# Optimization experiments

Hardware: AMD Instinct MI355X
Metric: run time of the kernel (lower is better)

The kernel has to match this reference:

```python
import jax, jax.numpy as jnp
import numpy as np

B = 4           # batchsize == poolsize, pool = arange(B)
N_NODES = 32768
N_EDGES = 262144
CH_V = 16
CH_E = 16
HID = 64
CH_MSG = 2 * CH_V + CH_E  # 48


def setup_inputs() -> dict:
    key = jax.random.key(0)
    ks = jax.random.split(key, 8)
    node_vals = jax.random.normal(ks[0], (B, N_NODES, CH_V), jnp.float32) * 0.01
    edge_vals = jax.random.normal(ks[1], (B, N_EDGES, CH_E), jnp.float32) * 0.1
    conn_a = jax.random.randint(ks[2], (N_EDGES,), 0, N_NODES)
    conn_b = jax.random.randint(ks[3], (N_EDGES,), 0, N_NODES)
    w = lambda k, sh: jax.random.normal(k, sh, jnp.float32) * 0.1
    return {
        "node_vals": node_vals, "edge_vals": edge_vals,
        "conn_a": conn_a, "conn_b": conn_b,
        "Wm1": w(ks[4], (CH_MSG, HID)), "bm1": jnp.zeros((HID,), jnp.float32),
        "Wm2": w(ks[5], (HID, CH_MSG)), "bm2": jnp.zeros((CH_MSG,), jnp.float32),
        "Wu1": w(ks[6], (3 * CH_V, HID)), "bu1": jnp.zeros((HID,), jnp.float32),
        "Wu2": w(ks[7], (HID, CH_V)), "bu2": jnp.zeros((CH_V,), jnp.float32),
    }


def reference(node_vals, edge_vals, conn_a, conn_b,
              Wm1, bm1, Wm2, bm2, Wu1, bu1, Wu2, bu2):
    # NeuralGraph.timestep with node_dropout_p = edge_dropout_p = 0 (masks are identity),
    # use_update=True, average_messages=True, nodes=True, edges=True.
    h_a = node_vals[:, conn_a]                      # [B, E, CH_V] gather at source nodes
    h_b = node_vals[:, conn_b]                      # [B, E, CH_V] gather at target nodes
    h = jnp.concatenate([h_a, h_b, edge_vals], -1)  # [B, E, 48]
    # message MLP (Linear -> tanh -> Linear)
    m = jnp.tanh(h @ Wm1 + bm1) @ Wm2 + bm2         # [B, E, 48]
    m_a = m[..., :CH_V]
    m_b = m[..., CH_V:2 * CH_V]
    m_ab = m[..., 2 * CH_V:]
    # scatter-add aggregation per node (index_add_ along node dim)
    agg_a = jnp.zeros((B, N_NODES, CH_V), m.dtype).at[:, conn_a].add(m_a)
    agg_b = jnp.zeros((B, N_NODES, CH_V), m.dtype).at[:, conn_b].add(m_b)
    # count-based averaging (counts clamped to >= 1, matching the buffer fixup)
    ones = jnp.ones((N_EDGES,), m.dtype)
    cnt_a = jnp.maximum(jax.ops.segment_sum(ones, conn_a, num_segments=N_NODES), 1.0)
    cnt_b = jnp.maximum(jax.ops.segment_sum(ones, conn_b, num_segments=N_NODES), 1.0)
    agg_a = agg_a / cnt_a[None, :, None]
    agg_b = agg_b / cnt_b[None, :, None]
    # update MLP
    u_in = jnp.concatenate([agg_a, agg_b, node_vals], -1)   # [B, N, 48]
    updates = jnp.tanh(u_in @ Wu1 + bu1) @ Wu2 + bu2        # [B, N, CH_V]
    new_node_vals = node_vals + updates
    new_edge_vals = edge_vals + m_ab
    return new_node_vals, new_edge_vals
```

## Files before the change

kernel.cpp:

```cpp
#include <hip/hip_runtime.h>
#include <hip/hip_bf16.h>
#include <cstdint>
#include <cstddef>

#define B 4
#define NN 32768
#define NE 262144
#define CV 16
#define CE 16
#define HID 64
#define CM 48

using frag  = __attribute__((ext_vector_type(8))) short;
using f32x4 = __attribute__((ext_vector_type(4))) float;

__device__ __forceinline__ float fast_tanh(float x) {
    float e = __expf(2.0f * x);
    return 1.0f - 2.0f / (e + 1.0f);
}

__device__ __forceinline__ unsigned short f2bf(float x) {
    union { float f; unsigned u; } v; v.f = x;
    unsigned r = (v.u + 0x7FFFu + ((v.u >> 16) & 1u)) >> 16;
    return (unsigned short)r;
}

__device__ __forceinline__ float bf2f(unsigned short x) {
    union { unsigned u; float f; } v; v.u = ((unsigned)x) << 16;
    return v.f;
}

__device__ __forceinline__ unsigned pk2bf(float lo, float hi) {
    union { __hip_bfloat162 h; unsigned u; } v;
    v.h = __float22bfloat162_rn(make_float2(lo, hi));
    return v.u;
}

__device__ __forceinline__ unsigned swo(int row, int byte_off) {
    return (unsigned)((row << 7) + (byte_off ^ ((row & 7) << 4)));
}

__device__ __forceinline__ void acc8(float* a, uint4 v) {
    a[0] += bf2f((unsigned short)(v.x & 0xFFFFu));
    a[1] += bf2f((unsigned short)(v.x >> 16));
    a[2] += bf2f((unsigned short)(v.y & 0xFFFFu));
    a[3] += bf2f((unsigned short)(v.y >> 16));
    a[4] += bf2f((unsigned short)(v.z & 0xFFFFu));
    a[5] += bf2f((unsigned short)(v.z >> 16));
    a[6] += bf2f((unsigned short)(v.w & 0xFFFFu));
    a[7] += bf2f((unsigned short)(v.w >> 16));
}

__global__ __launch_bounds__(256) void prep_kernel(
    const float* __restrict__ Wm1, const float* __restrict__ bm1,
    const float* __restrict__ Wm2,
    const float* __restrict__ Wu1, const float* __restrict__ bu1,
    const float* __restrict__ Wu2,
    const float* __restrict__ node_vals,
    unsigned short* __restrict__ pW1, unsigned short* __restrict__ pW2,
    unsigned short* __restrict__ pWu1, unsigned short* __restrict__ pWu2,
    unsigned short* __restrict__ nv16)
{
    int i = blockIdx.x * 256 + threadIdx.x;

    {
        int x0 = i * 8;
        const float4* src = (const float4*)(node_vals + x0);
        float4 v0 = src[0], v1 = src[1];
        uint4 o;
        o.x = pk2bf(v0.x, v0.y); o.y = pk2bf(v0.z, v0.w);
        o.z = pk2bf(v1.x, v1.y); o.w = pk2bf(v1.z, v1.w);
        *(uint4*)(nv16 + x0) = o;
    }

    if (blockIdx.x == 0) {
        for (int x = threadIdx.x; x < 4 * 2 * 64 * 8; x += 256) {
            int j = x & 7, lane = (x >> 3) & 63, ks = (x >> 9) & 1, mt = x >> 10;
            int m = mt * 16 + (lane & 15);
            int k = ks * 32 + (lane >> 4) * 8 + j;
            float w = (k < 48) ? Wm1[k * 64 + m] : (k == 48 ? bm1[m] : 0.0f);
            pW1[x] = f2bf(w);
        }
    } else if (blockIdx.x == 1) {
        for (int x = threadIdx.x; x < 3 * 2 * 64 * 8; x += 256) {
            int j = x & 7, lane = (x >> 3) & 63, ks = (x >> 9) & 1, mt = x >> 10;
            int m = mt * 16 + (lane & 15);
            int k = ks * 32 + (lane >> 4) * 8 + j;
            pW2[x] = f2bf(Wm2[k * 48 + m]);
        }
    } else if (blockIdx.x == 2) {
        for (int x = threadIdx.x; x < 4 * 2 * 64 * 8; x += 256) {
            int j = x & 7, lane = (x >> 3) & 63, ks = (x >> 9) & 1, mt = x >> 10;
            int m = mt * 16 + (lane & 15);
            int k = ks * 32 + (lane >> 4) * 8 + j;
            float w = (k < 48) ? Wu1[k * 64 + m] : (k == 48 ? bu1[m] : 0.0f);
            pWu1[x] = f2bf(w);
        }
    } else if (blockIdx.x == 3) {
        for (int x = threadIdx.x; x < 2 * 64 * 8; x += 256) {
            int j = x & 7, lane = (x >> 3) & 63, ks = x >> 9;
            int m = lane & 15;
            int k = ks * 32 + (lane >> 4) * 8 + j;
            pWu2[x] = f2bf(Wu2[k * 16 + m]);
        }
    }
}

__global__ __launch_bounds__(1024) void scan_kernel(
    const int* __restrict__ cnt_a, int* __restrict__ start_a,
    const int* __restrict__ cnt_b, int* __restrict__ start_b)
{
    const int* cnt = (blockIdx.x == 0) ? cnt_a : cnt_b;
    int* start     = (blockIdx.x == 0) ? start_a : start_b;

    __shared__ int sw[16];
    int t = threadIdx.x;
    int lane = t & 63;
    int wv   = t >> 6;
    int base = t * 32;

    int local[32];
    int sum = 0;
    const int4* p = (const int4*)(cnt + base);
#pragma unroll
    for (int q = 0; q < 8; q++) {
        int4 v = p[q];
        local[q*4+0] = v.x; local[q*4+1] = v.y; local[q*4+2] = v.z; local[q*4+3] = v.w;
        sum += v.x + v.y + v.z + v.w;
    }
    int inc = sum;
#pragma unroll
    for (int off = 1; off < 64; off <<= 1) {
        int u = __shfl_up(inc, off);
        if (lane >= off) inc += u;
    }
    if (lane == 63) sw[wv] = inc;
    __syncthreads();
    if (wv == 0 && lane < 16) {
        int v = sw[lane];
        int i2 = v;
#pragma unroll
        for (int off = 1; off < 16; off <<= 1) {
            int u = __shfl_up(i2, off);
            if (lane >= off) i2 += u;
        }
        sw[lane] = i2 - v;
    }
    __syncthreads();

    int run = sw[wv] + inc - sum;
    int4* ps = (int4*)(start + base);
#pragma unroll
    for (int q = 0; q < 8; q++) {
        int4 o;
        o.x = run; run += local[q*4+0];
        o.y = run; run += local[q*4+1];
        o.z = run; run += local[q*4+2];
        o.w = run; run += local[q*4+3];
        ps[q] = o;
    }
}

__global__ __launch_bounds__(256) void eidx_kernel(
    const int* __restrict__ ca, const int* __restrict__ cb,
    const int* __restrict__ rank_a, const int* __restrict__ rank_b,
    const int* __restrict__ start_a, const int* __restrict__ start_b,
    int* __restrict__ eidx_a, int* __restrict__ eidx_b)
{
    int e = blockIdx.x * 256 + threadIdx.x;
    eidx_a[start_a[ca[e]] + rank_a[e]] = e;
    eidx_b[start_b[cb[e]] + rank_b[e]] = e;
}

__global__ __launch_bounds__(256, 5) void edge_kernel(
    const unsigned short* __restrict__ nv16, const float* __restrict__ edge_vals,
    const int* __restrict__ ca, const int* __restrict__ cb,
    int* __restrict__ cnt_a, int* __restrict__ cnt_b,
    int* __restrict__ rank_a, int* __restrict__ rank_b,
    const unsigned short* __restrict__ pW1, const unsigned short* __restrict__ pW2,
    const float* __restrict__ bm2,
    float* __restrict__ out_edge,
    unsigned short* __restrict__ ma, unsigned short* __restrict__ mb)
{
    __shared__ unsigned short sH[256 * 64];
    char* sB = (char*)sH;

    int t    = threadIdx.x;
    int lane = t & 63;
    int col  = lane & 15;
    int quad = lane >> 4;
    int erow = (t >> 6) * 64;
    int cha  = quad * 4;

    size_t eb  = (size_t)blockIdx.x * 256;
    size_t idx = eb + t;
    int e  = (int)(idx & (NE - 1));
    int bb = (int)(idx >> 18);

    int na = ca[e], nb = cb[e];

    if (bb == 0) {
        rank_a[e] = atomicAdd(&cnt_a[na], 1);
        rank_b[e] = atomicAdd(&cnt_b[nb], 1);
    }

    {
        const uint4* gA = (const uint4*)(nv16 + ((size_t)bb * NN + na) * CV);
        const uint4* gB = (const uint4*)(nv16 + ((size_t)bb * NN + nb) * CV);
        uint4 a0 = gA[0], a1 = gA[1];
        uint4 b0 = gB[0], b1 = gB[1];
        const float4* pE = (const float4*)(edge_vals + idx * CE);
        float4 ev0 = pE[0], ev1 = pE[1], ev2 = pE[2], ev3 = pE[3];

        unsigned pk[32];
        *(uint4*)&pk[0]  = a0;  *(uint4*)&pk[4]  = a1;
        *(uint4*)&pk[8]  = b0;  *(uint4*)&pk[12] = b1;
        pk[16] = pk2bf(ev0.x, ev0.y); pk[17] = pk2bf(ev0.z, ev0.w);
        pk[18] = pk2bf(ev1.x, ev1.y); pk[19] = pk2bf(ev1.z, ev1.w);
        pk[20] = pk2bf(ev2.x, ev2.y); pk[21] = pk2bf(ev2.z, ev2.w);
        pk[22] = pk2bf(ev3.x, ev3.y); pk[23] = pk2bf(ev3.z, ev3.w);
        pk[24] = 0x3F80u;
#pragma unroll
        for (int q = 25; q < 32; q++) pk[q] = 0;
        const uint4* src = (const uint4*)pk;
#pragma unroll
        for (int q = 0; q < 8; q++)
            *(uint4*)(sB + swo(t, q * 16)) = src[q];
    }
    asm volatile("s_waitcnt lgkmcnt(0)" ::: "memory");

#pragma unroll
    for (int hh = 0; hh < 2; hh++) {
        int r0 = erow + hh * 32 + col;

        frag w1f[4][2];
#pragma unroll
        for (int mt = 0; mt < 4; mt++)
#pragma unroll
            for (int ks = 0; ks < 2; ks++)
                w1f[mt][ks] = *(const frag*)&pW1[(((mt * 2 + ks) * 64) + lane) * 8];

        f32x4 acc1[4][2];
#pragma unroll
        for (int mt = 0; mt < 4; mt++)
#pragma unroll
            for (int n = 0; n < 2; n++) acc1[mt][n] = (f32x4){0.f, 0.f, 0.f, 0.f};

#pragma unroll
        for (int ks = 0; ks < 2; ks++) {
            frag bfr[2];
#pragma unroll
            for (int n = 0; n < 2; n++)
                bfr[n] = *(const frag*)(sB + swo(r0 + n * 16, ks * 64 + quad * 16));
#pragma unroll
            for (int mt = 0; mt < 4; mt++)
#pragma unroll
                for (int n = 0; n < 2; n++)
                    acc1[mt][n] = __builtin_amdgcn_mfma_f32_16x16x32_bf16(
                        w1f[mt][ks], bfr[n], acc1[mt][n], 0, 0, 0);
        }

#pragma unroll
        for (int n = 0; n < 2; n++) {
            int row = r0 + n * 16;
#pragma unroll
            for (int mt = 0; mt < 4; mt++) {
                uint2 w;
                w.x = pk2bf(fast_tanh(acc1[mt][n][0]), fast_tanh(acc1[mt][n][1]));
                w.y = pk2bf(fast_tanh(acc1[mt][n][2]), fast_tanh(acc1[mt][n][3]));
                *(uint2*)(sB + swo(row, mt * 32 + quad * 8)) = w;
            }
        }
        asm volatile("s_waitcnt lgkmcnt(0)" ::: "memory");

        frag w2f[3][2];
#pragma unroll
        for (int mt = 0; mt < 3; mt++)
#pragma unroll
            for (int ks = 0; ks < 2; ks++)
                w2f[mt][ks] = *(const frag*)&pW2[(((mt * 2 + ks) * 64) + lane) * 8];

        f32x4 acc2[3][2];
#pragma unroll
        for (int mt = 0; mt < 3; mt++)
#pragma unroll
            for (int n = 0; n < 2; n++) acc2[mt][n] = (f32x4){0.f, 0.f, 0.f, 0.f};

#pragma unroll
        for (int ks = 0; ks < 2; ks++) {
            frag bfr[2];
#pragma unroll
            for (int n = 0; n < 2; n++)
                bfr[n] = *(const frag*)(sB + swo(r0 + n * 16, ks * 64 + quad * 16));
#pragma unroll
            for (int mt = 0; mt < 3; mt++)
#pragma unroll
                for (int n = 0; n < 2; n++)
                    acc2[mt][n] = __builtin_amdgcn_mfma_f32_16x16x32_bf16(
                        w2f[mt][ks], bfr[n], acc2[mt][n], 0, 0, 0);
        }

        float4 b2e = *(const float4*)&bm2[32 + cha];
#pragma unroll
        for (int n = 0; n < 2; n++) {
            int le = r0 + n * 16;
            size_t o = (eb + le) * CE + cha;
            float4 evv = *(const float4*)&edge_vals[o];
            float4 ov;
            ov.x = evv.x + acc2[2][n][0] + b2e.x;
            ov.y = evv.y + acc2[2][n][1] + b2e.y;
            ov.z = evv.z + acc2[2][n][2] + b2e.z;
            ov.w = evv.w + acc2[2][n][3] + b2e.w;
            *(float4*)&out_edge[o] = ov;
        }

        float4 b2a = *(const float4*)&bm2[cha];
        float4 b2b = *(const float4*)&bm2[16 + cha];
#pragma unroll
        for (int n = 0; n < 2; n++) {
            int row = r0 + n * 16;
            uint2 wa;
            wa.x = pk2bf(acc2[0][n][0] + b2a.x, acc2[0][n][1] + b2a.y);
            wa.y = pk2bf(acc2[0][n][2] + b2a.z, acc2[0][n][3] + b2a.w);
            *(uint2*)(sB + swo(row, quad * 8)) = wa;
            uint2 wb;
            wb.x = pk2bf(acc2[1][n][0] + b2b.x, acc2[1][n][1] + b2b.y);
            wb.y = pk2bf(acc2[1][n][2] + b2b.z, acc2[1][n][3] + b2b.w);
            *(uint2*)(sB + swo(row, 32 + quad * 8)) = wb;
        }
    }
    asm volatile("s_waitcnt lgkmcnt(0)" ::: "memory");

    {
        uint4 a0 = *(const uint4*)(sB + swo(t, 0));
        uint4 a1 = *(const uint4*)(sB + swo(t, 16));
        uint4 b0 = *(const uint4*)(sB + swo(t, 32));
        uint4 b1 = *(const uint4*)(sB + swo(t, 48));
        unsigned short* pa = &ma[idx * 16];
        *(uint4*)(pa + 0) = a0;
        *(uint4*)(pa + 8) = a1;
        unsigned short* pb = &mb[idx * 16];
        *(uint4*)(pb + 0) = b0;
        *(uint4*)(pb + 8) = b1;
    }
}

__global__ __launch_bounds__(256, 4) void node_kernel(
    const float* __restrict__ node_vals,
    const unsigned short* __restrict__ ma, const unsigned short* __restrict__ mb,
    const int* __restrict__ eidx_a, const int* __restrict__ eidx_b,
    const int* __restrict__ start_a, const int* __restrict__ start_b,
    const int* __restrict__ cnt_a, const int* __restrict__ cnt_b,
    const unsigned short* __restrict__ pWu1, const unsigned short* __restrict__ pWu2,
    const float* __restrict__ bu2,
    float* __restrict__ out_node)
{
    __shared__ unsigned short sH[256 * 64];
    char* sB = (char*)sH;

    int t    = threadIdx.x;
    int lane = t & 63;
    int col  = lane & 15;
    int quad = lane >> 4;
    int erow = (t >> 6) * 64;

    int g = blockIdx.x * 256 + t;
    int n = g & (NN - 1);
    int b = g >> 15;

    float4 pn[4];
    {
        float ua[16] = {0.f,0.f,0.f,0.f,0.f,0.f,0.f,0.f,0.f,0.f,0.f,0.f,0.f,0.f,0.f,0.f};
        float ub[16] = {0.f,0.f,0.f,0.f,0.f,0.f,0.f,0.f,0.f,0.f,0.f,0.f,0.f,0.f,0.f,0.f};
        int da = cnt_a[n], sa = start_a[n];
        int db = cnt_b[n], sbn = start_b[n];
        const int* ia = eidx_a + sa;
        const int* ib = eidx_b + sbn;
        const unsigned short* mab = ma + (size_t)b * NE * 16;
        const unsigned short* mbb = mb + (size_t)b * NE * 16;
        for (int k = 0; k < da; k++) {
            int ee = ia[k];
            const uint4* p = (const uint4*)(mab + (size_t)ee * 16);
            acc8(&ua[0], p[0]);
            acc8(&ua[8], p[1]);
        }
        for (int k = 0; k < db; k++) {
            int ee = ib[k];
            const uint4* p = (const uint4*)(mbb + (size_t)ee * 16);
            acc8(&ub[0], p[0]);
            acc8(&ub[8], p[1]);
        }
        float inva = 1.0f / (float)max(da, 1);
        float invb = 1.0f / (float)max(db, 1);

        const float4* pnv = (const float4*)(node_vals + (size_t)g * CV);
#pragma unroll
        for (int q = 0; q < 4; q++) pn[q] = pnv[q];

        unsigned pk[32];
#pragma unroll
        for (int q = 0; q < 8; q++)
            pk[q] = pk2bf(ua[2*q] * inva, ua[2*q+1] * inva);
#pragma unroll
        for (int q = 0; q < 8; q++)
            pk[8 + q] = pk2bf(ub[2*q] * invb, ub[2*q+1] * invb);
#pragma unroll
        for (int q = 0; q < 4; q++) {
            pk[16 + 2*q + 0] = pk2bf(pn[q].x, pn[q].y);
            pk[16 + 2*q + 1] = pk2bf(pn[q].z, pn[q].w);
        }
        pk[24] = 0x3F80u;
#pragma unroll
        for (int q = 25; q < 32; q++) pk[q] = 0;
        const uint4* src = (const uint4*)pk;
#pragma unroll
        for (int q = 0; q < 8; q++)
            *(uint4*)(sB + swo(t, q * 16)) = src[q];
    }
    asm volatile("s_waitcnt lgkmcnt(0)" ::: "memory");

#pragma unroll
    for (int hh = 0; hh < 2; hh++) {
        int r0 = erow + hh * 32 + col;

        frag w1f[4][2];
#pragma unroll
        for (int mt = 0; mt < 4; mt++)
#pragma unroll
            for (int ks = 0; ks < 2; ks++)
                w1f[mt][ks] = *(const frag*)&pWu1[(((mt * 2 + ks) * 64) + lane) * 8];

        f32x4 acc1[4][2];
#pragma unroll
        for (int mt = 0; mt < 4; mt++)
#pragma unroll
            for (int nt = 0; nt < 2; nt++) acc1[mt][nt] = (f32x4){0.f, 0.f, 0.f, 0.f};

#pragma unroll
        for (int ks = 0; ks < 2; ks++) {
            frag bfr[2];
#pragma unroll
            for (int nt = 0; nt < 2; nt++)
                bfr[nt] = *(const frag*)(sB + swo(r0 + nt * 16, ks * 64 + quad * 16));
#pragma unroll
            for (int mt = 0; mt < 4; mt++)
#pragma unroll
                for (int nt = 0; nt < 2; nt++)
                    acc1[mt][nt] = __builtin_amdgcn_mfma_f32_16x16x32_bf16(
                        w1f[mt][ks], bfr[nt], acc1[mt][nt], 0, 0, 0);
        }

#pragma unroll
        for (int nt = 0; nt < 2; nt++) {
            int row = r0 + nt * 16;
#pragma unroll
            for (int mt = 0; mt < 4; mt++) {
                uint2 w;
                w.x = pk2bf(fast_tanh(acc1[mt][nt][0]), fast_tanh(acc1[mt][nt][1]));
                w.y = pk2bf(fast_tanh(acc1[mt][nt][2]), fast_tanh(acc1[mt][nt][3]));
                *(uint2*)(sB + swo(row, mt * 32 + quad * 8)) = w;
            }
        }
        asm volatile("s_waitcnt lgkmcnt(0)" ::: "memory");

        frag w2f[2];
#pragma unroll
        for (int ks = 0; ks < 2; ks++)
            w2f[ks] = *(const frag*)&pWu2[(ks * 64 + lane) * 8];

        f32x4 acc2[2];
#pragma unroll
        for (int nt = 0; nt < 2; nt++) acc2[nt] = (f32x4){0.f, 0.f, 0.f, 0.f};

#pragma unroll
        for (int ks = 0; ks < 2; ks++) {
            frag bfr[2];
#pragma unroll
            for (int nt = 0; nt < 2; nt++)
                bfr[nt] = *(const frag*)(sB + swo(r0 + nt * 16, ks * 64 + quad * 16));
#pragma unroll
            for (int nt = 0; nt < 2; nt++)
                acc2[nt] = __builtin_amdgcn_mfma_f32_16x16x32_bf16(
                    w2f[ks], bfr[nt], acc2[nt], 0, 0, 0);
        }

#pragma unroll
        for (int nt = 0; nt < 2; nt++) {
            int row = r0 + nt * 16;
            float4 v;
            v.x = acc2[nt][0]; v.y = acc2[nt][1];
            v.z = acc2[nt][2]; v.w = acc2[nt][3];
            *(float4*)(sB + swo(row, 64 + quad * 16)) = v;
        }
    }
    asm volatile("s_waitcnt lgkmcnt(0)" ::: "memory");

    {
        const float4* pb2 = (const float4*)bu2;
        float4* po = (float4*)&out_node[(size_t)g * CV];
#pragma unroll
        for (int q = 0; q < 4; q++) {
            float4 m = *(const float4*)(sB + swo(t, 64 + q * 16));
            float4 c = pb2[q];
            float4 o;
            o.x = pn[q].x + m.x + c.x;
            o.y = pn[q].y + m.y + c.y;
            o.z = pn[q].z + m.z + c.z;
            o.w = pn[q].w + m.w + c.w;
            po[q] = o;
        }
    }
}

extern "C" void kernel_launch(void* const* d_in, const int* in_sizes, int n_in,
                              void* d_out, int out_size, void* d_ws, size_t ws_size,
                              hipStream_t stream) {
    const float* node_vals = (const float*)d_in[0];
    const float* edge_vals = (const float*)d_in[1];
    const int*   ca        = (const int*)d_in[2];
    const int*   cb        = (const int*)d_in[3];
    const float* Wm1 = (const float*)d_in[4];
    const float* bm1 = (const float*)d_in[5];
    const float* Wm2 = (const float*)d_in[6];
    const float* bm2 = (const float*)d_in[7];
    const float* Wu1 = (const float*)d_in[8];
    const float* bu1 = (const float*)d_in[9];
    const float* Wu2 = (const float*)d_in[10];
    const float* bu2 = (const float*)d_in[11];

    float* out_node = (float*)d_out;
    float* out_edge = out_node + (size_t)B * NN * CV;

    unsigned short* ma = (unsigned short*)d_ws;
    unsigned short* mb = ma + (size_t)B * NE * 16;
    int* cnt_a   = (int*)(mb + (size_t)B * NE * 16);
    int* cnt_b   = cnt_a + NN;
    int* start_a = cnt_b + NN;
    int* start_b = start_a + NN;
    int* rank_a  = start_b + NN;
    int* rank_b  = rank_a + NE;
    int* eidx_a  = rank_b + NE;
    int* eidx_b  = eidx_a + NE;
    unsigned short* pW1  = (unsigned short*)(eidx_b + NE);
    unsigned short* pW2  = pW1 + 4096;
    unsigned short* pWu1 = pW2 + 3072;
    unsigned short* pWu2 = pWu1 + 4096;
    unsigned short* nv16 = pWu2 + 1024;

    hipMemsetAsync(cnt_a, 0, 2 * (size_t)NN * sizeof(int), stream);

    prep_kernel<<<NE / 256, 256, 0, stream>>>(
        Wm1, bm1, Wm2, Wu1, bu1, Wu2, node_vals,
        pW1, pW2, pWu1, pWu2, nv16);
    edge_kernel<<<(B * NE) / 256, 256, 0, stream>>>(
        nv16, edge_vals, ca, cb, cnt_a, cnt_b, rank_a, rank_b,
        pW1, pW2, bm2, out_edge, ma, mb);
    scan_kernel<<<2, 1024, 0, stream>>>(cnt_a, start_a, cnt_b, start_b);
    eidx_kernel<<<NE / 256, 256, 0, stream>>>(
        ca, cb, rank_a, rank_b, start_a, start_b, eidx_a, eidx_b);
    node_kernel<<<(B * NN) / 256, 256, 0, stream>>>(
        node_vals, ma, mb, eidx_a, eidx_b, start_a, start_b, cnt_a, cnt_b,
        pWu1, pWu2, bu2, out_node);
}
```

Measured before the change: 288.6 us.

## Interleave batch in message buffers and map batches to waves per edge block

Moves the per-node degree counting and rank atomics out of the edge kernel into the prep kernel. Each edge block now covers 64 edges with one wave per batch, so the four batch copies share the ca/cb index loads. Message buffers switch to an edge-major, batch-interleaved layout, and node-kernel threads cover four batches of one node. The four threads gathering a node's messages therefore read one contiguous 128-byte span per edge instead of four scattered ones. The trade-off is more scattered node-value gathers per wave and a reordered kernel sequence.

```diff
diff --git a/kernel.cpp b/kernel.cpp
--- a/kernel.cpp
+++ b/kernel.cpp
@@ -51,7 +51,10 @@
     a[7] += bf2f((unsigned short)(v.w >> 16));
 }
 
-__global__ __launch_bounds__(256) void prep_kernel(
+__global__ __launch_bounds__(256) void count_kernel(
+    const int* __restrict__ ca, const int* __restrict__ cb,
+    int* __restrict__ cnt_a, int* __restrict__ cnt_b,
+    int* __restrict__ rank_a, int* __restrict__ rank_b,
     const float* __restrict__ Wm1, const float* __restrict__ bm1,
     const float* __restrict__ Wm2,
     const float* __restrict__ Wu1, const float* __restrict__ bu1,
@@ -62,6 +65,8 @@
     unsigned short* __restrict__ nv16)
 {
     int i = blockIdx.x * 256 + threadIdx.x;
+    rank_a[i] = atomicAdd(&cnt_a[ca[i]], 1);
+    rank_b[i] = atomicAdd(&cnt_b[cb[i]], 1);
 
     {
         int x0 = i * 8;
@@ -175,8 +180,6 @@
 __global__ __launch_bounds__(256, 5) void edge_kernel(
     const unsigned short* __restrict__ nv16, const float* __restrict__ edge_vals,
     const int* __restrict__ ca, const int* __restrict__ cb,
-    int* __restrict__ cnt_a, int* __restrict__ cnt_b,
-    int* __restrict__ rank_a, int* __restrict__ rank_b,
     const unsigned short* __restrict__ pW1, const unsigned short* __restrict__ pW2,
     const float* __restrict__ bm2,
     float* __restrict__ out_edge,
@@ -189,20 +192,16 @@
     int lane = t & 63;
     int col  = lane & 15;
     int quad = lane >> 4;
-    int erow = (t >> 6) * 64;
+    int wv   = t >> 6;
+    int erow = wv * 64;
     int cha  = quad * 4;
 
-    size_t eb  = (size_t)blockIdx.x * 256;
-    size_t idx = eb + t;
-    int e  = (int)(idx & (NE - 1));
-    int bb = (int)(idx >> 18);
+    int bid = blockIdx.x;
+    int e   = bid * 64 + lane;
+    int bb  = wv;
+    size_t idx = (size_t)bb * NE + e;
 
     int na = ca[e], nb = cb[e];
-
-    if (bb == 0) {
-        rank_a[e] = atomicAdd(&cnt_a[na], 1);
-        rank_b[e] = atomicAdd(&cnt_b[nb], 1);
-    }
 
     {
         const uint4* gA = (const uint4*)(nv16 + ((size_t)bb * NN + na) * CV);
@@ -303,8 +302,8 @@
         float4 b2e = *(const float4*)&bm2[32 + cha];
 #pragma unroll
         for (int n = 0; n < 2; n++) {
-            int le = r0 + n * 16;
-            size_t o = (eb + le) * CE + cha;
+            int row = r0 + n * 16;
+            size_t o = ((size_t)wv * NE + (size_t)bid * 64 + (row & 63)) * CE + cha;
             float4 evv = *(const float4*)&edge_vals[o];
             float4 ov;
             ov.x = evv.x + acc2[2][n][0] + b2e.x;
@@ -336,10 +335,11 @@
         uint4 a1 = *(const uint4*)(sB + swo(t, 16));
         uint4 b0 = *(const uint4*)(sB + swo(t, 32));
         uint4 b1 = *(const uint4*)(sB + swo(t, 48));
-        unsigned short* pa = &ma[idx * 16];
+        size_t mo = ((size_t)e * 4 + bb) * 16;
+        unsigned short* pa = &ma[mo];
         *(uint4*)(pa + 0) = a0;
         *(uint4*)(pa + 8) = a1;
-        unsigned short* pb = &mb[idx * 16];
+        unsigned short* pb = &mb[mo];
         *(uint4*)(pb + 0) = b0;
         *(uint4*)(pb + 8) = b1;
     }
@@ -364,9 +364,9 @@
     int quad = lane >> 4;
     int erow = (t >> 6) * 64;
 
-    int g = blockIdx.x * 256 + t;
-    int n = g & (NN - 1);
-    int b = g >> 15;
+    int b  = t & 3;
+    int n  = blockIdx.x * 64 + (t >> 2);
+    int g  = b * NN + n;
 
     float4 pn[4];
     {
@@ -376,17 +376,15 @@
         int db = cnt_b[n], sbn = start_b[n];
         const int* ia = eidx_a + sa;
         const int* ib = eidx_b + sbn;
-        const unsigned short* mab = ma + (size_t)b * NE * 16;
-        const unsigned short* mbb = mb + (size_t)b * NE * 16;
         for (int k = 0; k < da; k++) {
             int ee = ia[k];
-            const uint4* p = (const uint4*)(mab + (size_t)ee * 16);
+            const uint4* p = (const uint4*)(ma + ((size_t)ee * 4 + b) * 16);
             acc8(&ua[0], p[0]);
             acc8(&ua[8], p[1]);
         }
         for (int k = 0; k < db; k++) {
             int ee = ib[k];
-            const uint4* p = (const uint4*)(mbb + (size_t)ee * 16);
+            const uint4* p = (const uint4*)(mb + ((size_t)ee * 4 + b) * 16);
             acc8(&ub[0], p[0]);
             acc8(&ub[8], p[1]);
         }
@@ -532,8 +530,8 @@
     float* out_edge = out_node + (size_t)B * NN * CV;
 
     unsigned short* ma = (unsigned short*)d_ws;
-    unsigned short* mb = ma + (size_t)B * NE * 16;
-    int* cnt_a   = (int*)(mb + (size_t)B * NE * 16);
+    unsigned short* mb = ma + (size_t)NE * B * 16;
+    int* cnt_a   = (int*)(mb + (size_t)NE * B * 16);
     int* cnt_b   = cnt_a + NN;
     int* start_a = cnt_b + NN;
     int* start_b = start_a + NN;
@@ -549,16 +547,16 @@
 
     hipMemsetAsync(cnt_a, 0, 2 * (size_t)NN * sizeof(int), stream);
 
-    prep_kernel<<<NE / 256, 256, 0, stream>>>(
+    count_kernel<<<NE / 256, 256, 0, stream>>>(
+        ca, cb, cnt_a, cnt_b, rank_a, rank_b,
         Wm1, bm1, Wm2, Wu1, bu1, Wu2, node_vals,
         pW1, pW2, pWu1, pWu2, nv16);
-    edge_kernel<<<(B * NE) / 256, 256, 0, stream>>>(
-        nv16, edge_vals, ca, cb, cnt_a, cnt_b, rank_a, rank_b,
-        pW1, pW2, bm2, out_edge, ma, mb);
     scan_kernel<<<2, 1024, 0, stream>>>(cnt_a, start_a, cnt_b, start_b);
     eidx_kernel<<<NE / 256, 256, 0, stream>>>(
         ca, cb, rank_a, rank_b, start_a, start_b, eidx_a, eidx_b);
-    node_kernel<<<(B * NN) / 256, 256, 0, stream>>>(
+    edge_kernel<<<NE / 64, 256, 0, stream>>>(
+        nv16, edge_vals, ca, cb, pW1, pW2, bm2, out_edge, ma, mb);
+    node_kernel<<<NN / 64, 256, 0, stream>>>(
         node_vals, ma, mb, eidx_a, eidx_b, start_a, start_b, cnt_a, cnt_b,
         pWu1, pWu2, bu2, out_node);
 }
```

New measurement: 290.1 us. About the same (+0.5%).
